# Kernel tuning notes

Measured on AMD Instinct MI355X. Metric: run time of the kernel, lower is better.

The kernel has to match this reference:

```python
import jax, jax.numpy as jnp
import numpy as np

B, F, D = 4096, 512, 512


def setup_inputs() -> dict:
    key = jax.random.key(0)
    k1, k2, k3 = jax.random.split(key, 3)
    inputs = jax.random.normal(k1, (B, D), dtype=jnp.float32)
    mu = jax.random.normal(k2, (F, D), dtype=jnp.float32)        # exp_mu, random_normal init
    sigma = jax.random.normal(k3, (1, F, D), dtype=jnp.float32)  # exp_sigma, random_normal init
    temperature = jnp.array(2.0, dtype=jnp.float32)              # learned scalar, init 2.0
    return {"inputs": inputs, "mu": mu, "sigma": sigma, "temperature": temperature}


def reference(inputs, mu, sigma, temperature):
    # diff: [B, F, D] broadcast difference (the large fusable intermediate)
    diff = inputs[:, None, :] - mu[None, :, :]
    # scaled L2 norm over feature dim -> [B, F]
    dist = jnp.sqrt(jnp.sum(jnp.square(diff * sigma), axis=-1))
    loc = jnp.exp(-dist)
    # adaptive-temperature softmax gating over formulas
    return jax.nn.softmax(jax.nn.sigmoid(temperature) * loc, axis=-1)
```

## Files before the change

### kernel.cpp

```cpp
#include <hip/hip_runtime.h>
#include <hip/hip_bf16.h>
#include <stdint.h>

#define BB 4096
#define FF 512
#define DD 512
#define KDIM 1024

typedef __bf16 bf16x8 __attribute__((ext_vector_type(8)));
typedef float f32x4 __attribute__((ext_vector_type(4)));
typedef unsigned short u16x8 __attribute__((ext_vector_type(8)));

__device__ __forceinline__ unsigned short f2bf(float f) {
  unsigned u = __builtin_bit_cast(unsigned, f);
  u += 0x7FFFu + ((u >> 16) & 1u);
  return (unsigned short)(u >> 16);
}

__device__ __forceinline__ void async16(const void* g, void* l) {
  auto gp = reinterpret_cast<const __attribute__((address_space(1))) uint32_t*>(
      reinterpret_cast<uintptr_t>(g));
  auto lp = reinterpret_cast<__attribute__((address_space(3))) uint32_t*>(
      reinterpret_cast<uintptr_t>(l));
  __builtin_amdgcn_global_load_lds(gp, lp, 16, 0, 0);
}

__global__ __launch_bounds__(256) void prep_kernel(
    const float* __restrict__ x, const float* __restrict__ mu,
    const float* __restrict__ sg, unsigned short* __restrict__ A,
    unsigned short* __restrict__ W, float* __restrict__ c) {
  __shared__ float red[4];
  const int bid = blockIdx.x;
  const int t = threadIdx.x;
  if (bid < FF) {
    const int f = bid;
    float part = 0.f;
#pragma unroll
    for (int dd = 0; dd < 2; ++dd) {
      const int d = t + dd * 256;
      const float m = mu[f * DD + d];
      const float s = sg[f * DD + d];
      const float s2 = s * s;
      W[f * KDIM + d] = f2bf(s2);
      W[f * KDIM + DD + d] = f2bf(-2.f * s2 * m);
      part += s2 * m * m;
    }
#pragma unroll
    for (int off = 32; off > 0; off >>= 1) part += __shfl_down(part, off, 64);
    const int lane = t & 63, wave = t >> 6;
    if (lane == 0) red[wave] = part;
    __syncthreads();
    if (t == 0) c[f] = red[0] + red[1] + red[2] + red[3];
  } else {
    const int gid = (bid - FF) * 256 + t;
    const int i8 = gid * 8;
    const float4 v0 = *(const float4*)(x + i8);
    const float4 v1 = *(const float4*)(x + i8 + 4);
    const int b = i8 >> 9;
    const int d = i8 & 511;
    u16x8 q2, q1;
    q2[0] = f2bf(v0.x * v0.x); q2[1] = f2bf(v0.y * v0.y);
    q2[2] = f2bf(v0.z * v0.z); q2[3] = f2bf(v0.w * v0.w);
    q2[4] = f2bf(v1.x * v1.x); q2[5] = f2bf(v1.y * v1.y);
    q2[6] = f2bf(v1.z * v1.z); q2[7] = f2bf(v1.w * v1.w);
    q1[0] = f2bf(v0.x); q1[1] = f2bf(v0.y); q1[2] = f2bf(v0.z); q1[3] = f2bf(v0.w);
    q1[4] = f2bf(v1.x); q1[5] = f2bf(v1.y); q1[6] = f2bf(v1.z); q1[7] = f2bf(v1.w);
    *(u16x8*)(A + (size_t)b * KDIM + d) = q2;
    *(u16x8*)(A + (size_t)b * KDIM + DD + d) = q1;
  }
}

__global__ __launch_bounds__(256) void gemm_kernel(
    const unsigned short* __restrict__ A, const unsigned short* __restrict__ W,
    const float* __restrict__ c, float* __restrict__ out) {
  __shared__ __align__(16) unsigned short As[2][32 * 64];
  const int bid = blockIdx.x;
  const int xcd = bid & 7;
  const int l = bid >> 3;
  const int m0 = (xcd * 16 + (l & 15)) * 32;
  const int n0 = (l >> 4) * 64;
  const int tid = threadIdx.x;
  const int lane = tid & 63;
  const int wave = tid >> 6;

  f32x4 acc[2];
  acc[0] = (f32x4){0.f, 0.f, 0.f, 0.f};
  acc[1] = (f32x4){0.f, 0.f, 0.f, 0.f};

  const int srow = lane >> 3;
  const int sc16 = lane & 7;
  const int gcol = (sc16 ^ srow) * 8;
  const int quad = lane >> 4;
  const int r = lane & 15;

  const unsigned short* ag = A + (size_t)(m0 + wave * 8 + srow) * KDIM + gcol;
  const int arb = wave * 8 * 64;
  const unsigned short* wg0 = W + (size_t)(n0 + wave * 16 + r) * KDIM + quad * 8;

  async16(ag, &As[0][arb]);
  bf16x8 bc[2], bn[2];
  bc[0] = *(const bf16x8*)(wg0);
  bc[1] = *(const bf16x8*)(wg0 + 32);

  for (int kt = 0; kt < KDIM / 64; ++kt) {
    const int cur = kt & 1;
    __syncthreads();
    if (kt + 1 < KDIM / 64) {
      const int k1 = (kt + 1) * 64;
      async16(ag + k1, &As[cur ^ 1][arb]);
      bn[0] = *(const bf16x8*)(wg0 + k1);
      bn[1] = *(const bf16x8*)(wg0 + k1 + 32);
    }
#pragma unroll
    for (int kk = 0; kk < 2; ++kk) {
      const int pc = ((kk * 4 + quad) ^ (r & 7)) * 8;
#pragma unroll
      for (int mt = 0; mt < 2; ++mt) {
        bf16x8 a = *(const bf16x8*)&As[cur][(mt * 16 + r) * 64 + pc];
        acc[mt] = __builtin_amdgcn_mfma_f32_16x16x32_bf16(a, bc[kk], acc[mt], 0, 0, 0);
      }
    }
    bc[0] = bn[0];
    bc[1] = bn[1];
  }

  const int f = n0 + wave * 16 + r;
  const float cf = c[f];
#pragma unroll
  for (int mt = 0; mt < 2; ++mt) {
    const int mbase = m0 + mt * 16 + quad * 4;
#pragma unroll
    for (int rr = 0; rr < 4; ++rr) {
      const float d2 = acc[mt][rr] + cf;
      const float loc = __expf(-sqrtf(fmaxf(d2, 0.f)));
      out[(size_t)(mbase + rr) * FF + f] = loc;
    }
  }
}

__global__ __launch_bounds__(256) void softmax_kernel(
    float* __restrict__ out, const float* __restrict__ temp) {
  const int lane = threadIdx.x & 63;
  const int wave = threadIdx.x >> 6;
  const int row = blockIdx.x * 4 + wave;
  const float s = 1.f / (1.f + __expf(-temp[0]));
  float4* p = (float4*)(out + (size_t)row * FF + lane * 8);
  const float4 v0 = p[0];
  const float4 v1 = p[1];
  float l[8] = {v0.x * s, v0.y * s, v0.z * s, v0.w * s,
                v1.x * s, v1.y * s, v1.z * s, v1.w * s};
  float mx = l[0];
#pragma unroll
  for (int i = 1; i < 8; ++i) mx = fmaxf(mx, l[i]);
#pragma unroll
  for (int off = 32; off > 0; off >>= 1) mx = fmaxf(mx, __shfl_xor(mx, off, 64));
  float e[8], sum = 0.f;
#pragma unroll
  for (int i = 0; i < 8; ++i) { e[i] = __expf(l[i] - mx); sum += e[i]; }
#pragma unroll
  for (int off = 32; off > 0; off >>= 1) sum += __shfl_xor(sum, off, 64);
  const float inv = 1.f / sum;
  float4 w0 = {e[0] * inv, e[1] * inv, e[2] * inv, e[3] * inv};
  float4 w1 = {e[4] * inv, e[5] * inv, e[6] * inv, e[7] * inv};
  p[0] = w0; p[1] = w1;
}

__global__ __launch_bounds__(256) void naive_loc(
    const float* __restrict__ x, const float* __restrict__ mu,
    const float* __restrict__ sg, float* __restrict__ out) {
  __shared__ float xs[DD];
  const int b = blockIdx.x;
  for (int d = threadIdx.x; d < DD; d += 256) xs[d] = x[(size_t)b * DD + d];
  __syncthreads();
  for (int f = threadIdx.x; f < FF; f += 256) {
    float acc = 0.f;
    for (int d = 0; d < DD; ++d) {
      const float s = sg[(size_t)f * DD + d];
      const float df = (xs[d] - mu[(size_t)f * DD + d]) * s;
      acc = fmaf(df, df, acc);
    }
    out[(size_t)b * FF + f] = __expf(-sqrtf(acc));
  }
}

extern "C" void kernel_launch(void* const* d_in, const int* in_sizes, int n_in,
                              void* d_out, int out_size, void* d_ws, size_t ws_size,
                              hipStream_t stream) {
  const float* x = (const float*)d_in[0];
  const float* mu = (const float*)d_in[1];
  const float* sg = (const float*)d_in[2];
  const float* temp = (const float*)d_in[3];
  float* out = (float*)d_out;

  const size_t needA = (size_t)BB * KDIM * 2;
  const size_t needW = (size_t)FF * KDIM * 2;
  const size_t needC = (size_t)FF * 4;
  if (ws_size >= needA + needW + needC) {
    unsigned short* A = (unsigned short*)d_ws;
    unsigned short* W = A + (size_t)BB * KDIM;
    float* c = (float*)(W + (size_t)FF * KDIM);
    prep_kernel<<<FF + (BB * DD / 8) / 256, 256, 0, stream>>>(x, mu, sg, A, W, c);
    gemm_kernel<<<1024, 256, 0, stream>>>(A, W, c, out);
  } else {
    naive_loc<<<BB, 256, 0, stream>>>(x, mu, sg, out);
  }
  softmax_kernel<<<BB / 4, 256, 0, stream>>>(out, temp);
}
```

Before: 94.22 us.

## Fuse bf16 prep into GEMM staging and drop workspace round-trip

Removes the separate prep kernel that wrote bf16-expanded A and W matrices plus the c vector to workspace. The GEMM now loads fp32 x, sigma and mu directly and converts them to bf16 (squared or scaled) while staging into LDS. The per-formula constant c is reduced in-block through LDS. This saves a kernel launch and the workspace write and read traffic. In exchange each block redoes the conversions and re-reads fp32 mu and sigma, and the plain register loads replace the async global-to-LDS copies.

```diff
diff --git a/kernel.cpp b/kernel.cpp
--- a/kernel.cpp
+++ b/kernel.cpp
@@ -5,7 +5,6 @@
 #define BB 4096
 #define FF 512
 #define DD 512
-#define KDIM 1024
 
 typedef __bf16 bf16x8 __attribute__((ext_vector_type(8)));
 typedef float f32x4 __attribute__((ext_vector_type(4)));
@@ -17,63 +16,13 @@
   return (unsigned short)(u >> 16);
 }
 
-__device__ __forceinline__ void async16(const void* g, void* l) {
-  auto gp = reinterpret_cast<const __attribute__((address_space(1))) uint32_t*>(
-      reinterpret_cast<uintptr_t>(g));
-  auto lp = reinterpret_cast<__attribute__((address_space(3))) uint32_t*>(
-      reinterpret_cast<uintptr_t>(l));
-  __builtin_amdgcn_global_load_lds(gp, lp, 16, 0, 0);
-}
+__global__ __launch_bounds__(256) void gemm_fused_nws(
+    const float* __restrict__ x, const float* __restrict__ mu,
+    const float* __restrict__ sg, float* __restrict__ out) {
+  __shared__ __align__(16) unsigned short As[2][32 * 64];
+  __shared__ __align__(16) unsigned short Ws[2][64 * 64];
+  __shared__ float cLds[64][4];
 
-__global__ __launch_bounds__(256) void prep_kernel(
-    const float* __restrict__ x, const float* __restrict__ mu,
-    const float* __restrict__ sg, unsigned short* __restrict__ A,
-    unsigned short* __restrict__ W, float* __restrict__ c) {
-  __shared__ float red[4];
-  const int bid = blockIdx.x;
-  const int t = threadIdx.x;
-  if (bid < FF) {
-    const int f = bid;
-    float part = 0.f;
-#pragma unroll
-    for (int dd = 0; dd < 2; ++dd) {
-      const int d = t + dd * 256;
-      const float m = mu[f * DD + d];
-      const float s = sg[f * DD + d];
-      const float s2 = s * s;
-      W[f * KDIM + d] = f2bf(s2);
-      W[f * KDIM + DD + d] = f2bf(-2.f * s2 * m);
-      part += s2 * m * m;
-    }
-#pragma unroll
-    for (int off = 32; off > 0; off >>= 1) part += __shfl_down(part, off, 64);
-    const int lane = t & 63, wave = t >> 6;
-    if (lane == 0) red[wave] = part;
-    __syncthreads();
-    if (t == 0) c[f] = red[0] + red[1] + red[2] + red[3];
-  } else {
-    const int gid = (bid - FF) * 256 + t;
-    const int i8 = gid * 8;
-    const float4 v0 = *(const float4*)(x + i8);
-    const float4 v1 = *(const float4*)(x + i8 + 4);
-    const int b = i8 >> 9;
-    const int d = i8 & 511;
-    u16x8 q2, q1;
-    q2[0] = f2bf(v0.x * v0.x); q2[1] = f2bf(v0.y * v0.y);
-    q2[2] = f2bf(v0.z * v0.z); q2[3] = f2bf(v0.w * v0.w);
-    q2[4] = f2bf(v1.x * v1.x); q2[5] = f2bf(v1.y * v1.y);
-    q2[6] = f2bf(v1.z * v1.z); q2[7] = f2bf(v1.w * v1.w);
-    q1[0] = f2bf(v0.x); q1[1] = f2bf(v0.y); q1[2] = f2bf(v0.z); q1[3] = f2bf(v0.w);
-    q1[4] = f2bf(v1.x); q1[5] = f2bf(v1.y); q1[6] = f2bf(v1.z); q1[7] = f2bf(v1.w);
-    *(u16x8*)(A + (size_t)b * KDIM + d) = q2;
-    *(u16x8*)(A + (size_t)b * KDIM + DD + d) = q1;
-  }
-}
-
-__global__ __launch_bounds__(256) void gemm_kernel(
-    const unsigned short* __restrict__ A, const unsigned short* __restrict__ W,
-    const float* __restrict__ c, float* __restrict__ out) {
-  __shared__ __align__(16) unsigned short As[2][32 * 64];
   const int bid = blockIdx.x;
   const int xcd = bid & 7;
   const int l = bid >> 3;
@@ -82,50 +31,104 @@
   const int tid = threadIdx.x;
   const int lane = tid & 63;
   const int wave = tid >> 6;
+  const int quad = lane >> 4;
+  const int r = lane & 15;
 
   f32x4 acc[2];
   acc[0] = (f32x4){0.f, 0.f, 0.f, 0.f};
   acc[1] = (f32x4){0.f, 0.f, 0.f, 0.f};
+  float cacc = 0.f;
 
-  const int srow = lane >> 3;
-  const int sc16 = lane & 7;
-  const int gcol = (sc16 ^ srow) * 8;
-  const int quad = lane >> 4;
-  const int r = lane & 15;
+  const int arow = tid >> 3;
+  const int ac8 = tid & 7;
+  const int wf = tid >> 2;
+  const int wdo = (tid & 3) * 16;
 
-  const unsigned short* ag = A + (size_t)(m0 + wave * 8 + srow) * KDIM + gcol;
-  const int arb = wave * 8 * 64;
-  const unsigned short* wg0 = W + (size_t)(n0 + wave * 16 + r) * KDIM + quad * 8;
+  auto stage = [&](int buf, int skt) {
+    const int dbase = (skt & 7) * 64;
+    {
+      const float* xp = x + (size_t)(m0 + arow) * DD + dbase + ac8 * 8;
+      const float4 v0 = ((const float4*)xp)[0];
+      const float4 v1 = ((const float4*)xp)[1];
+      u16x8 q;
+      if (skt < 8) {
+        q[0] = f2bf(v0.x * v0.x); q[1] = f2bf(v0.y * v0.y);
+        q[2] = f2bf(v0.z * v0.z); q[3] = f2bf(v0.w * v0.w);
+        q[4] = f2bf(v1.x * v1.x); q[5] = f2bf(v1.y * v1.y);
+        q[6] = f2bf(v1.z * v1.z); q[7] = f2bf(v1.w * v1.w);
+      } else {
+        q[0] = f2bf(v0.x); q[1] = f2bf(v0.y); q[2] = f2bf(v0.z); q[3] = f2bf(v0.w);
+        q[4] = f2bf(v1.x); q[5] = f2bf(v1.y); q[6] = f2bf(v1.z); q[7] = f2bf(v1.w);
+      }
+      *(u16x8*)&As[buf][arow * 64 + ((ac8 ^ (arow & 7)) * 8)] = q;
+    }
+    {
+      const float* sgp = sg + (size_t)(n0 + wf) * DD + dbase + wdo;
+      const float4 s0 = ((const float4*)sgp)[0];
+      const float4 s1 = ((const float4*)sgp)[1];
+      const float4 s2 = ((const float4*)sgp)[2];
+      const float4 s3 = ((const float4*)sgp)[3];
+      u16x8 o0, o1;
+      if (skt < 8) {
+        o0[0] = f2bf(s0.x * s0.x); o0[1] = f2bf(s0.y * s0.y);
+        o0[2] = f2bf(s0.z * s0.z); o0[3] = f2bf(s0.w * s0.w);
+        o0[4] = f2bf(s1.x * s1.x); o0[5] = f2bf(s1.y * s1.y);
+        o0[6] = f2bf(s1.z * s1.z); o0[7] = f2bf(s1.w * s1.w);
+        o1[0] = f2bf(s2.x * s2.x); o1[1] = f2bf(s2.y * s2.y);
+        o1[2] = f2bf(s2.z * s2.z); o1[3] = f2bf(s2.w * s2.w);
+        o1[4] = f2bf(s3.x * s3.x); o1[5] = f2bf(s3.y * s3.y);
+        o1[6] = f2bf(s3.z * s3.z); o1[7] = f2bf(s3.w * s3.w);
+      } else {
+        const float* mup = mu + (size_t)(n0 + wf) * DD + dbase + wdo;
+        const float4 m0v = ((const float4*)mup)[0];
+        const float4 m1v = ((const float4*)mup)[1];
+        const float4 m2v = ((const float4*)mup)[2];
+        const float4 m3v = ((const float4*)mup)[3];
+        float sv[16] = {s0.x, s0.y, s0.z, s0.w, s1.x, s1.y, s1.z, s1.w,
+                        s2.x, s2.y, s2.z, s2.w, s3.x, s3.y, s3.z, s3.w};
+        float mv[16] = {m0v.x, m0v.y, m0v.z, m0v.w, m1v.x, m1v.y, m1v.z, m1v.w,
+                        m2v.x, m2v.y, m2v.z, m2v.w, m3v.x, m3v.y, m3v.z, m3v.w};
+        unsigned short ow[16];
+#pragma unroll
+        for (int i = 0; i < 16; ++i) {
+          const float s2e = sv[i] * sv[i];
+          ow[i] = f2bf(-2.f * s2e * mv[i]);
+          cacc = fmaf(s2e * mv[i], mv[i], cacc);
+        }
+#pragma unroll
+        for (int i = 0; i < 8; ++i) { o0[i] = ow[i]; o1[i] = ow[i + 8]; }
+      }
+      unsigned short* wb = &Ws[buf][wf * 64];
+      const int c0 = (tid & 3) * 2;
+      *(u16x8*)&wb[((c0) ^ (wf & 7)) * 8] = o0;
+      *(u16x8*)&wb[((c0 + 1) ^ (wf & 7)) * 8] = o1;
+    }
+  };
 
-  async16(ag, &As[0][arb]);
-  bf16x8 bc[2], bn[2];
-  bc[0] = *(const bf16x8*)(wg0);
-  bc[1] = *(const bf16x8*)(wg0 + 32);
+  stage(0, 0);
 
-  for (int kt = 0; kt < KDIM / 64; ++kt) {
+  for (int kt = 0; kt < 16; ++kt) {
     const int cur = kt & 1;
     __syncthreads();
-    if (kt + 1 < KDIM / 64) {
-      const int k1 = (kt + 1) * 64;
-      async16(ag + k1, &As[cur ^ 1][arb]);
-      bn[0] = *(const bf16x8*)(wg0 + k1);
-      bn[1] = *(const bf16x8*)(wg0 + k1 + 32);
-    }
+    if (kt < 15) stage(cur ^ 1, kt + 1);
 #pragma unroll
     for (int kk = 0; kk < 2; ++kk) {
       const int pc = ((kk * 4 + quad) ^ (r & 7)) * 8;
+      bf16x8 b = *(const bf16x8*)&Ws[cur][(wave * 16 + r) * 64 + pc];
 #pragma unroll
       for (int mt = 0; mt < 2; ++mt) {
         bf16x8 a = *(const bf16x8*)&As[cur][(mt * 16 + r) * 64 + pc];
-        acc[mt] = __builtin_amdgcn_mfma_f32_16x16x32_bf16(a, bc[kk], acc[mt], 0, 0, 0);
+        acc[mt] = __builtin_amdgcn_mfma_f32_16x16x32_bf16(a, b, acc[mt], 0, 0, 0);
       }
     }
-    bc[0] = bn[0];
-    bc[1] = bn[1];
   }
 
-  const int f = n0 + wave * 16 + r;
-  const float cf = c[f];
+  cLds[wf][tid & 3] = cacc;
+  __syncthreads();
+
+  const int fl = wave * 16 + r;
+  const float cf = cLds[fl][0] + cLds[fl][1] + cLds[fl][2] + cLds[fl][3];
+  const int f = n0 + fl;
 #pragma unroll
   for (int mt = 0; mt < 2; ++mt) {
     const int mbase = m0 + mt * 16 + quad * 4;
@@ -138,7 +141,7 @@
   }
 }
 
-__global__ __launch_bounds__(256) void softmax_kernel(
+__global__ __launch_bounds__(256) void softmax_inplace(
     float* __restrict__ out, const float* __restrict__ temp) {
   const int lane = threadIdx.x & 63;
   const int wave = threadIdx.x >> 6;
@@ -165,24 +168,6 @@
   p[0] = w0; p[1] = w1;
 }
 
-__global__ __launch_bounds__(256) void naive_loc(
-    const float* __restrict__ x, const float* __restrict__ mu,
-    const float* __restrict__ sg, float* __restrict__ out) {
-  __shared__ float xs[DD];
-  const int b = blockIdx.x;
-  for (int d = threadIdx.x; d < DD; d += 256) xs[d] = x[(size_t)b * DD + d];
-  __syncthreads();
-  for (int f = threadIdx.x; f < FF; f += 256) {
-    float acc = 0.f;
-    for (int d = 0; d < DD; ++d) {
-      const float s = sg[(size_t)f * DD + d];
-      const float df = (xs[d] - mu[(size_t)f * DD + d]) * s;
-      acc = fmaf(df, df, acc);
-    }
-    out[(size_t)b * FF + f] = __expf(-sqrtf(acc));
-  }
-}
-
 extern "C" void kernel_launch(void* const* d_in, const int* in_sizes, int n_in,
                               void* d_out, int out_size, void* d_ws, size_t ws_size,
                               hipStream_t stream) {
@@ -191,18 +176,8 @@
   const float* sg = (const float*)d_in[2];
   const float* temp = (const float*)d_in[3];
   float* out = (float*)d_out;
+  (void)d_ws; (void)ws_size;
 
-  const size_t needA = (size_t)BB * KDIM * 2;
-  const size_t needW = (size_t)FF * KDIM * 2;
-  const size_t needC = (size_t)FF * 4;
-  if (ws_size >= needA + needW + needC) {
-    unsigned short* A = (unsigned short*)d_ws;
-    unsigned short* W = A + (size_t)BB * KDIM;
-    float* c = (float*)(W + (size_t)FF * KDIM);
-    prep_kernel<<<FF + (BB * DD / 8) / 256, 256, 0, stream>>>(x, mu, sg, A, W, c);
-    gemm_kernel<<<1024, 256, 0, stream>>>(A, W, c, out);
-  } else {
-    naive_loc<<<BB, 256, 0, stream>>>(x, mu, sg, out);
-  }
-  softmax_kernel<<<BB / 4, 256, 0, stream>>>(out, temp);
+  gemm_fused_nws<<<1024, 256, 0, stream>>>(x, mu, sg, out);
+  softmax_inplace<<<BB / 4, 256, 0, stream>>>(out, temp);
 }
```

New measurement: 100.9 us. +7.1%, slower.
